# Kernel tuning notes

Hardware: AMD Instinct MI355X
Metric: run time of the kernel (lower is better)

Reference implementation:

```python
import jax, jax.numpy as jnp
import numpy as np

N_TOKENS = 8192
TOP_K = 2
N_EXPERTS = 8
D_IN = 2048
D_OUT = 2048


def setup_inputs() -> dict:
    key = jax.random.key(0)
    k1, k2, k3, k4 = jax.random.split(key, 4)
    inputs = jax.random.normal(k1, (N_TOKENS, D_IN), dtype=jnp.float32)
    # stored as [E, out, in], matching nn.Parameter(torch.empty(E, output_size, input_size))
    expert_weights = 0.02 * jax.random.normal(k2, (N_EXPERTS, D_OUT, D_IN), dtype=jnp.float32)
    gates = jax.nn.softmax(jax.random.normal(k3, (N_TOKENS, TOP_K), dtype=jnp.float32), axis=-1)
    # per (token, slot) expert assignment, then sort by expert as the router would
    flat_experts = jax.random.randint(k4, (N_TOKENS * TOP_K,), 0, N_EXPERTS, dtype=jnp.int32)
    sorted_scattered_idxs = jnp.argsort(flat_experts).astype(jnp.int32)
    sorted_expert_idxs = flat_experts[sorted_scattered_idxs]
    expert_offsets = jnp.cumsum(jnp.bincount(flat_experts, length=N_EXPERTS)).astype(jnp.int32)
    return {
        "inputs": inputs,
        "expert_weights": expert_weights,
        "gates": gates,
        "k": TOP_K,
        "sorted_expert_idxs": sorted_expert_idxs,
        "sorted_scattered_idxs": sorted_scattered_idxs,
        "expert_offsets": expert_offsets,
    }


def reference(inputs, expert_weights, gates, k, sorted_expert_idxs, sorted_scattered_idxs, expert_offsets):
    N, d_in = inputs.shape
    E = expert_weights.shape[0]
    Nk = N * k
    # forward permutes weight [E, out, in] -> [E, in, out]
    W = jnp.transpose(expert_weights, (0, 2, 1))
    d_out = W.shape[-1]
    # invert the sort: expert id for each flat (token, slot) index
    expert_per_flat = jnp.zeros((Nk,), dtype=sorted_expert_idxs.dtype).at[
        sorted_scattered_idxs].set(sorted_expert_idxs)
    # scatter2scatter: out_flat[j] = x[j // k] @ W[expert_per_flat[j]]
    x_rep = jnp.repeat(inputs, k, axis=0)  # [N*k, d_in]
    out_flat = jnp.zeros((Nk, d_out), dtype=inputs.dtype)
    for e in range(E):  # small fixed expert count; masked grouped GEMM
        mask = (expert_per_flat == e)[:, None]
        out_flat = out_flat + jnp.where(mask, x_rep, 0.0) @ W[e]
    # combine: (gates.unsqueeze(1) @ output_expanded).squeeze(1)
    out = jnp.einsum('nk,nkd->nd', gates, out_flat.reshape(N, k, d_out))
    return out
```

## Files before the change

kernel.cpp:

```cpp
#include <hip/hip_runtime.h>
#include <hip/hip_bf16.h>
#include <stdint.h>

#define NTOK   8192
#define TOPK   2
#define NEXP   8
#define DIN    2048
#define DOUT   2048
#define NK     (NTOK*TOPK)

typedef __bf16 bf16_8 __attribute__((ext_vector_type(8)));
typedef float  f32x4  __attribute__((ext_vector_type(4)));

__device__ __forceinline__ void gl2lds16(const void* g, void* l) {
  auto gp = reinterpret_cast<const __attribute__((address_space(1))) uint32_t*>(
      reinterpret_cast<uintptr_t>(g));
  auto lp = reinterpret_cast<__attribute__((address_space(3))) uint32_t*>(
      reinterpret_cast<uintptr_t>(l));
  __builtin_amdgcn_global_load_lds(gp, lp, 16, 0, 0);
}

__global__ void cvt_f32_bf16(const float4* __restrict__ src,
                             uint4* __restrict__ dst, int n8) {
  int i = blockIdx.x * 256 + threadIdx.x;
  if (i >= n8) return;
  float4 a = src[2 * i];
  float4 b = src[2 * i + 1];
  union { __bf16 h[8]; uint4 u; } r;
  r.h[0] = (__bf16)a.x; r.h[1] = (__bf16)a.y; r.h[2] = (__bf16)a.z; r.h[3] = (__bf16)a.w;
  r.h[4] = (__bf16)b.x; r.h[5] = (__bf16)b.y; r.h[6] = (__bf16)b.z; r.h[7] = (__bf16)b.w;
  dst[i] = r.u;
}

__global__ __launch_bounds__(256, 4)
void moe_gemm(const __bf16* __restrict__ X,
              const __bf16* __restrict__ W,
              const int* __restrict__ ssi,
              const int* __restrict__ offs,
              __bf16* __restrict__ flat)
{
  __shared__ __bf16 lA[128 * 32];
  __shared__ __bf16 lB[128 * 32];
  __shared__ int   sTok[128];
  __shared__ int   sF[128];

  const int tid = threadIdx.x;
  const int bid = blockIdx.x;
  const int nt  = bid & 15;
  const int mtg = bid >> 4;

  int start = 0, end = 0, e, cum = 0, prev = 0, mloc = 0, found = 0;
  for (e = 0; e < NEXP; ++e) {
    int oe  = offs[e];
    int seg = oe - prev;
    int t   = (seg + 127) >> 7;
    if (mtg < cum + t) { start = prev; end = oe; mloc = mtg - cum; found = 1; break; }
    cum += t; prev = oe;
  }
  if (!found) return;

  const int m0 = start + mloc * 128;

  if (tid < 128) {
    int p     = m0 + tid;
    int valid = p < end;
    int f     = ssi[valid ? p : (end - 1)];
    sTok[tid] = f >> 1;
    sF[tid]   = valid ? f : -1;
  }
  __syncthreads();

  const int rs = tid >> 2;
  const int kc = tid & 3;
  const __bf16* pA0 = X + (size_t)sTok[rs]      * DIN + kc * 8;
  const __bf16* pA1 = X + (size_t)sTok[rs + 64] * DIN + kc * 8;
  const __bf16* wB  = W + (size_t)e * DOUT * DIN + (size_t)(nt * 128) * DIN;
  const __bf16* pB0 = wB + (size_t)rs        * DIN + kc * 8;
  const __bf16* pB1 = wB + (size_t)(rs + 64) * DIN + kc * 8;
  char* ldsAb = (char*)lA + (tid & 192) * 16;
  char* ldsBb = (char*)lB + (tid & 192) * 16;

  const int w  = tid >> 6;
  const int l  = tid & 63;
  const int wm = w >> 1, wn = w & 1;
  const int lr = l & 15;
  const int kq = l >> 4;
  const __bf16* aBase = lA + (wm * 64 + lr) * 32 + kq * 8;
  const __bf16* bBase = lB + (wn * 64 + lr) * 32 + kq * 8;

  f32x4 acc[4][4] = {};

  for (int it = 0; it < DIN / 32; ++it) {
    __syncthreads();
    gl2lds16(pA0, ldsAb);
    gl2lds16(pA1, ldsAb + 4096);
    gl2lds16(pB0, ldsBb);
    gl2lds16(pB1, ldsBb + 4096);
    pA0 += 32; pA1 += 32; pB0 += 32; pB1 += 32;
    __syncthreads();

    bf16_8 af[4], bf[4];
#pragma unroll
    for (int am = 0; am < 4; ++am) af[am] = *(const bf16_8*)(aBase + am * 512);
#pragma unroll
    for (int bn = 0; bn < 4; ++bn) bf[bn] = *(const bf16_8*)(bBase + bn * 512);
#pragma unroll
    for (int am = 0; am < 4; ++am)
#pragma unroll
      for (int bn = 0; bn < 4; ++bn)
        acc[am][bn] = __builtin_amdgcn_mfma_f32_16x16x32_bf16(
            af[am], bf[bn], acc[am][bn], 0, 0, 0);
  }

  const int colBase = nt * 128 + wn * 64 + lr;
  const int rq = kq * 4;
#pragma unroll
  for (int am = 0; am < 4; ++am) {
#pragma unroll
    for (int v = 0; v < 4; ++v) {
      int rl = wm * 64 + am * 16 + rq + v;
      int f  = sF[rl];
      if (f < 0) continue;
      __bf16* row = flat + (size_t)f * DOUT + colBase;
#pragma unroll
      for (int bn = 0; bn < 4; ++bn)
        row[bn * 16] = (__bf16)acc[am][bn][v];
    }
  }
}

__global__ __launch_bounds__(256)
void combine(const __bf16* __restrict__ flat, const float* __restrict__ gates,
             float* __restrict__ out) {
  const int n = blockIdx.x;
  const int c = threadIdx.x * 8;
  bf16_8 y0 = *(const bf16_8*)(flat + (size_t)(2 * n)     * DOUT + c);
  bf16_8 y1 = *(const bf16_8*)(flat + (size_t)(2 * n + 1) * DOUT + c);
  const float g0 = gates[2 * n];
  const float g1 = gates[2 * n + 1];
  float o[8];
#pragma unroll
  for (int j = 0; j < 8; ++j)
    o[j] = g0 * (float)y0[j] + g1 * (float)y1[j];
  float4* dst = (float4*)(out + (size_t)n * DOUT + c);
  dst[0] = *(float4*)&o[0];
  dst[1] = *(float4*)&o[4];
}

extern "C" void kernel_launch(void* const* d_in, const int* in_sizes, int n_in,
                              void* d_out, int out_size, void* d_ws, size_t ws_size,
                              hipStream_t stream) {
  const float* inputs = (const float*)d_in[0];
  const float* ew     = (const float*)d_in[1];
  const float* gates  = (const float*)d_in[2];
  const int*   ssi    = (const int*)d_in[5];
  const int*   offs   = (const int*)d_in[6];
  float* out = (float*)d_out;

  __bf16* wsW = (__bf16*)d_ws;
  __bf16* wsX = wsW + (size_t)NEXP * DOUT * DIN;
  __bf16* wsF = wsX + (size_t)NTOK * DIN;

  const int n8w = NEXP * DOUT * DIN / 8;
  const int n8x = NTOK * DIN / 8;
  cvt_f32_bf16<<<n8w / 256, 256, 0, stream>>>((const float4*)ew, (uint4*)wsW, n8w);
  cvt_f32_bf16<<<n8x / 256, 256, 0, stream>>>((const float4*)inputs, (uint4*)wsX, n8x);

  moe_gemm<<<136 * 16, 256, 0, stream>>>(wsX, wsW, ssi, offs, wsF);
  combine<<<NTOK, 256, 0, stream>>>(wsF, gates, out);
}
```

Measured before the change: 462.4 us.

## Double-buffer LDS tiles in MoE GEMM and fuse conversion kernels

The grouped GEMM now keeps two LDS buffers for the A and B tiles. The next K-slice is prefetched with global_load_lds while the MFMA work runs on the current slice, which cuts the barriers per iteration from two to one. The two f32-to-bf16 conversion launches are merged into one grid, and the combine kernel loads both gates with a single float2 read. The change doubles tile LDS usage, which could limit how many blocks fit per CU. The barrier's implicit wait on outstanding loads still bounds how much of the load latency is hidden.

```diff
diff --git a/kernel.cpp b/kernel.cpp
--- a/kernel.cpp
+++ b/kernel.cpp
@@ -20,15 +20,20 @@
   __builtin_amdgcn_global_load_lds(gp, lp, 16, 0, 0);
 }
 
-__global__ void cvt_f32_bf16(const float4* __restrict__ src,
-                             uint4* __restrict__ dst, int n8) {
-  int i = blockIdx.x * 256 + threadIdx.x;
-  if (i >= n8) return;
-  float4 a = src[2 * i];
-  float4 b = src[2 * i + 1];
+__global__ void cvt_all(const float4* __restrict__ w, uint4* __restrict__ wD,
+                        const float4* __restrict__ x, uint4* __restrict__ xD,
+                        int nW) {
+  int b = blockIdx.x;
+  const float4* src;
+  uint4* dst;
+  int i;
+  if (b < nW) { src = w; dst = wD; i = b * 256 + threadIdx.x; }
+  else        { src = x; dst = xD; i = (b - nW) * 256 + threadIdx.x; }
+  float4 a0 = src[2 * i];
+  float4 a1 = src[2 * i + 1];
   union { __bf16 h[8]; uint4 u; } r;
-  r.h[0] = (__bf16)a.x; r.h[1] = (__bf16)a.y; r.h[2] = (__bf16)a.z; r.h[3] = (__bf16)a.w;
-  r.h[4] = (__bf16)b.x; r.h[5] = (__bf16)b.y; r.h[6] = (__bf16)b.z; r.h[7] = (__bf16)b.w;
+  r.h[0] = (__bf16)a0.x; r.h[1] = (__bf16)a0.y; r.h[2] = (__bf16)a0.z; r.h[3] = (__bf16)a0.w;
+  r.h[4] = (__bf16)a1.x; r.h[5] = (__bf16)a1.y; r.h[6] = (__bf16)a1.z; r.h[7] = (__bf16)a1.w;
   dst[i] = r.u;
 }
 
@@ -39,8 +44,8 @@
               const int* __restrict__ offs,
               __bf16* __restrict__ flat)
 {
-  __shared__ __bf16 lA[128 * 32];
-  __shared__ __bf16 lB[128 * 32];
+  __shared__ __bf16 lA[2][128 * 32];
+  __shared__ __bf16 lB[2][128 * 32];
   __shared__ int   sTok[128];
   __shared__ int   sF[128];
 
@@ -85,25 +90,38 @@
   const int wm = w >> 1, wn = w & 1;
   const int lr = l & 15;
   const int kq = l >> 4;
-  const __bf16* aBase = lA + (wm * 64 + lr) * 32 + kq * 8;
-  const __bf16* bBase = lB + (wn * 64 + lr) * 32 + kq * 8;
+  const __bf16* aBase = (const __bf16*)lA + (wm * 64 + lr) * 32 + kq * 8;
+  const __bf16* bBase = (const __bf16*)lB + (wn * 64 + lr) * 32 + kq * 8;
+
+  gl2lds16(pA0, ldsAb);
+  gl2lds16(pA1, ldsAb + 4096);
+  gl2lds16(pB0, ldsBb);
+  gl2lds16(pB1, ldsBb + 4096);
+  pA0 += 32; pA1 += 32; pB0 += 32; pB1 += 32;
 
   f32x4 acc[4][4] = {};
 
   for (int it = 0; it < DIN / 32; ++it) {
+    const int cur = it & 1;
     __syncthreads();
-    gl2lds16(pA0, ldsAb);
-    gl2lds16(pA1, ldsAb + 4096);
-    gl2lds16(pB0, ldsBb);
-    gl2lds16(pB1, ldsBb + 4096);
-    pA0 += 32; pA1 += 32; pB0 += 32; pB1 += 32;
-    __syncthreads();
+    if (it < DIN / 32 - 1) {
+      const int nb = cur ^ 1;
+      char* a = ldsAb + nb * 8192;
+      char* b = ldsBb + nb * 8192;
+      gl2lds16(pA0, a);
+      gl2lds16(pA1, a + 4096);
+      gl2lds16(pB0, b);
+      gl2lds16(pB1, b + 4096);
+      pA0 += 32; pA1 += 32; pB0 += 32; pB1 += 32;
+    }
 
+    const __bf16* aB = aBase + cur * 4096;
+    const __bf16* bB = bBase + cur * 4096;
     bf16_8 af[4], bf[4];
 #pragma unroll
-    for (int am = 0; am < 4; ++am) af[am] = *(const bf16_8*)(aBase + am * 512);
+    for (int am = 0; am < 4; ++am) af[am] = *(const bf16_8*)(aB + am * 512);
 #pragma unroll
-    for (int bn = 0; bn < 4; ++bn) bf[bn] = *(const bf16_8*)(bBase + bn * 512);
+    for (int bn = 0; bn < 4; ++bn) bf[bn] = *(const bf16_8*)(bB + bn * 512);
 #pragma unroll
     for (int am = 0; am < 4; ++am)
 #pragma unroll
@@ -136,12 +154,11 @@
   const int c = threadIdx.x * 8;
   bf16_8 y0 = *(const bf16_8*)(flat + (size_t)(2 * n)     * DOUT + c);
   bf16_8 y1 = *(const bf16_8*)(flat + (size_t)(2 * n + 1) * DOUT + c);
-  const float g0 = gates[2 * n];
-  const float g1 = gates[2 * n + 1];
+  const float2 g = *(const float2*)(gates + 2 * n);
   float o[8];
 #pragma unroll
   for (int j = 0; j < 8; ++j)
-    o[j] = g0 * (float)y0[j] + g1 * (float)y1[j];
+    o[j] = g.x * (float)y0[j] + g.y * (float)y1[j];
   float4* dst = (float4*)(out + (size_t)n * DOUT + c);
   dst[0] = *(float4*)&o[0];
   dst[1] = *(float4*)&o[4];
@@ -163,8 +180,9 @@
 
   const int n8w = NEXP * DOUT * DIN / 8;
   const int n8x = NTOK * DIN / 8;
-  cvt_f32_bf16<<<n8w / 256, 256, 0, stream>>>((const float4*)ew, (uint4*)wsW, n8w);
-  cvt_f32_bf16<<<n8x / 256, 256, 0, stream>>>((const float4*)inputs, (uint4*)wsX, n8x);
+  const int nWb = n8w / 256, nXb = n8x / 256;
+  cvt_all<<<nWb + nXb, 256, 0, stream>>>((const float4*)ew, (uint4*)wsW,
+                                         (const float4*)inputs, (uint4*)wsX, nWb);
 
   moe_gemm<<<136 * 16, 256, 0, stream>>>(wsX, wsW, ssi, offs, wsF);
   combine<<<NTOK, 256, 0, stream>>>(wsF, gates, out);
```

Result: no change. 454.8 us (-1.6%).
